# Optimization experiments

Hardware: AMD Instinct MI355X
Metric: run time of the kernel (lower is better)

The kernel has to match this reference:

```python
import jax, jax.numpy as jnp
import numpy as np

B = 128          # batch
H = 4            # input_size (number of local blocks / heads)
SEQ = 256        # seq_length
E = 64           # embedding_size
D = 64           # qkv_size
LH = SEQ // H    # seq_length_head = 64
NEG = -1e20

def setup_inputs() -> dict:
    key = jax.random.key(0)
    ks = jax.random.split(key, 7)
    scale = 0.02
    sequence = jax.random.normal(ks[0], (B, SEQ, E), dtype=jnp.float32)
    WQ = jax.random.normal(ks[1], (H, LH * D, LH * E), dtype=jnp.float32) * scale
    WK = jax.random.normal(ks[2], (H, LH * D, LH * E), dtype=jnp.float32) * scale
    WV = jax.random.normal(ks[3], (H, LH * D, LH * E), dtype=jnp.float32) * scale
    bQ = jax.random.normal(ks[4], (H, LH * D), dtype=jnp.float32) * scale
    bK = jax.random.normal(ks[5], (H, LH * D), dtype=jnp.float32) * scale
    bV = jax.random.normal(ks[6], (H, LH * D), dtype=jnp.float32) * scale
    return {"sequence": sequence, "WQ": WQ, "bQ": bQ, "WK": WK, "bK": bK, "WV": WV, "bV": bV}

def reference(sequence, WQ, bQ, WK, bK, WV, bV):
    b = sequence.shape[0]
    # split sequence into H independent local blocks, flatten each block
    x = sequence.reshape(b, H, LH * E)  # [B, H, Lh*E]
    # per-block dense projections (flattened linears, as in the original)
    Q = (jnp.einsum('bhi,hoi->bho', x, WQ) + bQ).reshape(b, H, LH, D)
    K = (jnp.einsum('bhi,hoi->bho', x, WK) + bK).reshape(b, H, LH, D)
    V = (jnp.einsum('bhi,hoi->bho', x, WV) + bV).reshape(b, H, LH, D)
    scores = jnp.einsum('bhqd,bhkd->bhqk', Q, K)  # [B, H, Lh, Lh]
    # masked=True: add -1e20 above the diagonal (as in torch.triu(..., diagonal=1))
    mask = jnp.triu(jnp.full((LH, LH), NEG, dtype=scores.dtype), k=1)
    scores = scores + mask
    # FAITHFUL to original: nn.Softmax(dim=1) on [B, Lh, Lh] -> softmax over QUERY axis
    attn = jax.nn.softmax(scores, axis=2)
    Z = jnp.einsum('bhqk,bhkd->bhqd', attn, V) * (1.0 / jnp.sqrt(jnp.float32(D)))
    return Z.reshape(b, SEQ, D)
```

## Files before the change

kernel.cpp:

```cpp
#include <hip/hip_runtime.h>

typedef _Float16 half8 __attribute__((ext_vector_type(8)));
typedef float floatx16 __attribute__((ext_vector_type(16)));

#define B_   128
#define H_   4
#define SEQ_ 256
#define E_   64
#define D_   64
#define LH_  64
#define IN_  (LH_*E_)
#define OUT_ (LH_*D_)
#define QKV_MAT_ELEMS (B_*H_*OUT_)

__global__ __launch_bounds__(256, 3) void qkv_gemm(
    const float* __restrict__ seq,
    const float* __restrict__ WQ, const float* __restrict__ bQ,
    const float* __restrict__ WK, const float* __restrict__ bK,
    const float* __restrict__ WV, const float* __restrict__ bV,
    _Float16* __restrict__ qkv)
{
    const int o0  = blockIdx.x * 64;
    const int h   = blockIdx.y;
    const int mat = blockIdx.z;
    const float* __restrict__ W    = (mat == 0) ? WQ : (mat == 1) ? WK : WV;
    const float* __restrict__ bias = (mat == 0) ? bQ : (mat == 1) ? bK : bV;

    __shared__ half8 Xs[128 * 8];
    __shared__ half8 Wt[64 * 8];

    const int t    = threadIdx.x;
    const int wave = t >> 6;
    const int lane = t & 63;
    const int lrow = lane & 31;
    const int kg   = lane >> 5;

    floatx16 acc0, acc1;
    #pragma unroll
    for (int i = 0; i < 16; ++i) { acc0[i] = 0.f; acc1[i] = 0.f; }

    const size_t wbase = (size_t)h * IN_ * OUT_;

    for (int kt = 0; kt < 64; ++kt) {
        const int k0 = kt * 64;
        #pragma unroll
        for (int i = 0; i < 4; ++i) {
            int lin = t + 256 * i;
            int r = lin >> 3, k8 = lin & 7;
            const float* src = seq + (size_t)r * (SEQ_*E_) + (size_t)h * IN_ + k0 + k8 * 8;
            float4 f0 = ((const float4*)src)[0];
            float4 f1 = ((const float4*)src)[1];
            half8 v;
            v[0] = (_Float16)f0.x; v[1] = (_Float16)f0.y;
            v[2] = (_Float16)f0.z; v[3] = (_Float16)f0.w;
            v[4] = (_Float16)f1.x; v[5] = (_Float16)f1.y;
            v[6] = (_Float16)f1.z; v[7] = (_Float16)f1.w;
            Xs[r * 8 + (k8 ^ (r & 7))] = v;
        }
        #pragma unroll
        for (int i = 0; i < 2; ++i) {
            int lin = t + 256 * i;
            int r = lin >> 3, k8 = lin & 7;
            const float* src = W + wbase + (size_t)(o0 + r) * IN_ + k0 + k8 * 8;
            float4 f0 = ((const float4*)src)[0];
            float4 f1 = ((const float4*)src)[1];
            half8 v;
            v[0] = (_Float16)f0.x; v[1] = (_Float16)f0.y;
            v[2] = (_Float16)f0.z; v[3] = (_Float16)f0.w;
            v[4] = (_Float16)f1.x; v[5] = (_Float16)f1.y;
            v[6] = (_Float16)f1.z; v[7] = (_Float16)f1.w;
            Wt[r * 8 + (k8 ^ (r & 7))] = v;
        }
        __syncthreads();

        const int arow = wave * 32 + lrow;
        #pragma unroll
        for (int s = 0; s < 4; ++s) {
            int k8i = s * 2 + kg;
            half8 a  = Xs[arow * 8 + (k8i ^ (arow & 7))];
            half8 b0 = Wt[lrow * 8 + (k8i ^ (lrow & 7))];
            half8 b1 = Wt[(lrow + 32) * 8 + (k8i ^ (lrow & 7))];
            acc0 = __builtin_amdgcn_mfma_f32_32x32x16_f16(a, b0, acc0, 0, 0, 0);
            acc1 = __builtin_amdgcn_mfma_f32_32x32x16_f16(a, b1, acc1, 0, 0, 0);
        }
        __syncthreads();
    }

    const float bv0 = bias[(size_t)h * OUT_ + o0 + lrow];
    const float bv1 = bias[(size_t)h * OUT_ + o0 + 32 + lrow];
    _Float16* dst = qkv + (size_t)mat * QKV_MAT_ELEMS;
    #pragma unroll
    for (int r = 0; r < 16; ++r) {
        int row = (r & 3) + 8 * (r >> 2) + 4 * kg;
        int b   = wave * 32 + row;
        size_t idx = ((size_t)(b * H_ + h)) * OUT_ + o0;
        dst[idx + lrow]      = (_Float16)(acc0[r] + bv0);
        dst[idx + 32 + lrow] = (_Float16)(acc1[r] + bv1);
    }
}

__global__ __launch_bounds__(256, 2) void local_attn(
    const _Float16* __restrict__ qkv, float* __restrict__ out)
{
    __shared__ float Qs[64 * 65];
    __shared__ float Ks[64 * 65];
    __shared__ float Vs[64 * 65];
    __shared__ float Ss[64 * 65];

    const int t = threadIdx.x;
    const int h = blockIdx.x;
    const int b = blockIdx.y;
    const size_t base = ((size_t)(b * H_ + h)) * OUT_;

    #pragma unroll
    for (int i = 0; i < 2; ++i) {
        int unit = t + 256 * i;
        int q = unit >> 3, d8 = unit & 7;
        half8 vq = *(const half8*)(qkv + base + q * 64 + d8 * 8);
        half8 vk = *(const half8*)(qkv + (size_t)QKV_MAT_ELEMS + base + q * 64 + d8 * 8);
        half8 vv = *(const half8*)(qkv + (size_t)2 * QKV_MAT_ELEMS + base + q * 64 + d8 * 8);
        #pragma unroll
        for (int j = 0; j < 8; ++j) {
            Qs[q * 65 + d8 * 8 + j] = (float)vq[j];
            Ks[q * 65 + d8 * 8 + j] = (float)vk[j];
            Vs[q * 65 + d8 * 8 + j] = (float)vv[j];
        }
    }
    __syncthreads();

    const int w = t >> 6, lane = t & 63;

    {
        float kr[64];
        #pragma unroll
        for (int d = 0; d < 64; ++d) kr[d] = Ks[lane * 65 + d];
        #pragma unroll 2
        for (int qi = 0; qi < 16; ++qi) {
            int q = w * 16 + qi;
            float s = 0.f;
            #pragma unroll
            for (int d = 0; d < 64; ++d) s += Qs[q * 65 + d] * kr[d];
            if (lane > q) s = -1e20f;
            Ss[q * 65 + lane] = s;
        }
    }
    __syncthreads();

    if (t < 64) {
        const int k = t;
        float m = -3.4e38f;
        for (int q = 0; q < 64; ++q) m = fmaxf(m, Ss[q * 65 + k]);
        float sum = 0.f;
        for (int q = 0; q < 64; ++q) {
            float e = __expf(Ss[q * 65 + k] - m);
            Ss[q * 65 + k] = e;
            sum += e;
        }
        float inv = 1.f / sum;
        for (int q = 0; q < 64; ++q) Ss[q * 65 + k] *= inv;
    }
    __syncthreads();

    {
        float vr[64];
        #pragma unroll
        for (int k = 0; k < 64; ++k) vr[k] = Vs[k * 65 + lane];
        #pragma unroll 2
        for (int qi = 0; qi < 16; ++qi) {
            int q = w * 16 + qi;
            float z = 0.f;
            #pragma unroll
            for (int k = 0; k < 64; ++k) z += Ss[q * 65 + k] * vr[k];
            out[((size_t)b * SEQ_ + h * LH_ + q) * D_ + lane] = z * 0.125f;
        }
    }
}

extern "C" void kernel_launch(void* const* d_in, const int* in_sizes, int n_in,
                              void* d_out, int out_size, void* d_ws, size_t ws_size,
                              hipStream_t stream)
{
    const float* seq = (const float*)d_in[0];
    const float* WQ  = (const float*)d_in[1];
    const float* bQ  = (const float*)d_in[2];
    const float* WK  = (const float*)d_in[3];
    const float* bK  = (const float*)d_in[4];
    const float* WV  = (const float*)d_in[5];
    const float* bV  = (const float*)d_in[6];
    _Float16* qkv = (_Float16*)d_ws;
    float* out = (float*)d_out;

    dim3 g1(64, H_, 3);
    qkv_gemm<<<g1, 256, 0, stream>>>(seq, WQ, bQ, WK, bK, WV, bV, qkv);
    dim3 g2(H_, B_);
    local_attn<<<g2, 256, 0, stream>>>(qkv, out);
}
```

Measured before the change: 805.9 us.

## Load GEMM operands directly to registers and use MFMA in local attention

New measurement: 956.1 us. 18.6% more time.

```diff
diff --git a/kernel.cpp b/kernel.cpp
--- a/kernel.cpp
+++ b/kernel.cpp
@@ -13,77 +13,68 @@
 #define OUT_ (LH_*D_)
 #define QKV_MAT_ELEMS (B_*H_*OUT_)
 
-__global__ __launch_bounds__(256, 3) void qkv_gemm(
+__device__ __forceinline__ half8 cvt8(float4 lo, float4 hi) {
+    half8 v;
+    v[0] = (_Float16)lo.x; v[1] = (_Float16)lo.y;
+    v[2] = (_Float16)lo.z; v[3] = (_Float16)lo.w;
+    v[4] = (_Float16)hi.x; v[5] = (_Float16)hi.y;
+    v[6] = (_Float16)hi.z; v[7] = (_Float16)hi.w;
+    return v;
+}
+
+__global__ __launch_bounds__(128) void qkv_gemm(
     const float* __restrict__ seq,
     const float* __restrict__ WQ, const float* __restrict__ bQ,
     const float* __restrict__ WK, const float* __restrict__ bK,
     const float* __restrict__ WV, const float* __restrict__ bV,
     _Float16* __restrict__ qkv)
 {
-    const int o0  = blockIdx.x * 64;
-    const int h   = blockIdx.y;
-    const int mat = blockIdx.z;
+    const int i   = blockIdx.x;
+    const int h   = (i >> 1) & 3;
+    const int sub = (i & 1) + ((i >> 3) << 1);
+    const int mat = sub >> 6;
+    const int nt  = sub & 63;
+    const int o0  = nt * 64;
+
     const float* __restrict__ W    = (mat == 0) ? WQ : (mat == 1) ? WK : WV;
     const float* __restrict__ bias = (mat == 0) ? bQ : (mat == 1) ? bK : bV;
 
-    __shared__ half8 Xs[128 * 8];
-    __shared__ half8 Wt[64 * 8];
-
-    const int t    = threadIdx.x;
-    const int wave = t >> 6;
-    const int lane = t & 63;
+    const int wave = threadIdx.x >> 6;
+    const int lane = threadIdx.x & 63;
     const int lrow = lane & 31;
     const int kg   = lane >> 5;
-
-    floatx16 acc0, acc1;
-    #pragma unroll
-    for (int i = 0; i < 16; ++i) { acc0[i] = 0.f; acc1[i] = 0.f; }
-
-    const size_t wbase = (size_t)h * IN_ * OUT_;
+    const int m0   = wave * 64;
+
+    const float* xr0 = seq + (size_t)(m0 + lrow) * (SEQ_*E_) + (size_t)h * IN_ + kg * 8;
+    const float* xr1 = xr0 + (size_t)32 * (SEQ_*E_);
+    const float* wr0 = W + (size_t)h * IN_ * OUT_ + (size_t)(o0 + lrow) * IN_ + kg * 8;
+    const float* wr1 = wr0 + (size_t)32 * IN_;
+
+    floatx16 acc00, acc01, acc10, acc11;
+    #pragma unroll
+    for (int r = 0; r < 16; ++r) { acc00[r]=0.f; acc01[r]=0.f; acc10[r]=0.f; acc11[r]=0.f; }
 
     for (int kt = 0; kt < 64; ++kt) {
-        const int k0 = kt * 64;
-        #pragma unroll
-        for (int i = 0; i < 4; ++i) {
-            int lin = t + 256 * i;
-            int r = lin >> 3, k8 = lin & 7;
-            const float* src = seq + (size_t)r * (SEQ_*E_) + (size_t)h * IN_ + k0 + k8 * 8;
-            float4 f0 = ((const float4*)src)[0];
-            float4 f1 = ((const float4*)src)[1];
-            half8 v;
-            v[0] = (_Float16)f0.x; v[1] = (_Float16)f0.y;
-            v[2] = (_Float16)f0.z; v[3] = (_Float16)f0.w;
-            v[4] = (_Float16)f1.x; v[5] = (_Float16)f1.y;
-            v[6] = (_Float16)f1.z; v[7] = (_Float16)f1.w;
-            Xs[r * 8 + (k8 ^ (r & 7))] = v;
-        }
-        #pragma unroll
-        for (int i = 0; i < 2; ++i) {
-            int lin = t + 256 * i;
-            int r = lin >> 3, k8 = lin & 7;
-            const float* src = W + wbase + (size_t)(o0 + r) * IN_ + k0 + k8 * 8;
-            float4 f0 = ((const float4*)src)[0];
-            float4 f1 = ((const float4*)src)[1];
-            half8 v;
-            v[0] = (_Float16)f0.x; v[1] = (_Float16)f0.y;
-            v[2] = (_Float16)f0.z; v[3] = (_Float16)f0.w;
-            v[4] = (_Float16)f1.x; v[5] = (_Float16)f1.y;
-            v[6] = (_Float16)f1.z; v[7] = (_Float16)f1.w;
-            Wt[r * 8 + (k8 ^ (r & 7))] = v;
-        }
-        __syncthreads();
-
-        const int arow = wave * 32 + lrow;
         #pragma unroll
         for (int s = 0; s < 4; ++s) {
-            int k8i = s * 2 + kg;
-            half8 a  = Xs[arow * 8 + (k8i ^ (arow & 7))];
-            half8 b0 = Wt[lrow * 8 + (k8i ^ (lrow & 7))];
-            half8 b1 = Wt[(lrow + 32) * 8 + (k8i ^ (lrow & 7))];
-            acc0 = __builtin_amdgcn_mfma_f32_32x32x16_f16(a, b0, acc0, 0, 0, 0);
-            acc1 = __builtin_amdgcn_mfma_f32_32x32x16_f16(a, b1, acc1, 0, 0, 0);
-        }
-        __syncthreads();
+            const int k = kt * 64 + s * 16;
+            float4 a0l = *(const float4*)(xr0 + k);
+            float4 a0h = *(const float4*)(xr0 + k + 4);
+            float4 a1l = *(const float4*)(xr1 + k);
+            float4 a1h = *(const float4*)(xr1 + k + 4);
+            float4 b0l = *(const float4*)(wr0 + k);
+            float4 b0h = *(const float4*)(wr0 + k + 4);
+            float4 b1l = *(const float4*)(wr1 + k);
+            float4 b1h = *(const float4*)(wr1 + k + 4);
+            half8 a0 = cvt8(a0l, a0h);
+            half8 a1 = cvt8(a1l, a1h);
+            half8 b0 = cvt8(b0l, b0h);
+            half8 b1 = cvt8(b1l, b1h);
+            acc00 = __builtin_amdgcn_mfma_f32_32x32x16_f16(a0, b0, acc00, 0, 0, 0);
+            acc01 = __builtin_amdgcn_mfma_f32_32x32x16_f16(a0, b1, acc01, 0, 0, 0);
+            acc10 = __builtin_amdgcn_mfma_f32_32x32x16_f16(a1, b0, acc10, 0, 0, 0);
+            acc11 = __builtin_amdgcn_mfma_f32_32x32x16_f16(a1, b1, acc11, 0, 0, 0);
+        }
     }
 
     const float bv0 = bias[(size_t)h * OUT_ + o0 + lrow];
@@ -91,88 +82,127 @@
     _Float16* dst = qkv + (size_t)mat * QKV_MAT_ELEMS;
     #pragma unroll
     for (int r = 0; r < 16; ++r) {
-        int row = (r & 3) + 8 * (r >> 2) + 4 * kg;
-        int b   = wave * 32 + row;
-        size_t idx = ((size_t)(b * H_ + h)) * OUT_ + o0;
-        dst[idx + lrow]      = (_Float16)(acc0[r] + bv0);
-        dst[idx + 32 + lrow] = (_Float16)(acc1[r] + bv1);
-    }
-}
-
-__global__ __launch_bounds__(256, 2) void local_attn(
+        const int row = (r & 3) + 8 * (r >> 2) + 4 * kg;
+        const int b0r = m0 + row;
+        const int b1r = m0 + 32 + row;
+        size_t i0 = ((size_t)(b0r * H_ + h)) * OUT_ + o0;
+        size_t i1 = ((size_t)(b1r * H_ + h)) * OUT_ + o0;
+        dst[i0 + lrow]      = (_Float16)(acc00[r] + bv0);
+        dst[i0 + 32 + lrow] = (_Float16)(acc01[r] + bv1);
+        dst[i1 + lrow]      = (_Float16)(acc10[r] + bv0);
+        dst[i1 + 32 + lrow] = (_Float16)(acc11[r] + bv1);
+    }
+}
+
+__global__ __launch_bounds__(256) void local_attn(
     const _Float16* __restrict__ qkv, float* __restrict__ out)
 {
-    __shared__ float Qs[64 * 65];
-    __shared__ float Ks[64 * 65];
-    __shared__ float Vs[64 * 65];
-    __shared__ float Ss[64 * 65];
+    __shared__ half8 Pf[64 * 8];
+    __shared__ half8 Vt[64 * 8];
+    __shared__ float redM[2][64];
+    __shared__ float redS[2][64];
+    __shared__ float invL[64];
 
     const int t = threadIdx.x;
     const int h = blockIdx.x;
     const int b = blockIdx.y;
     const size_t base = ((size_t)(b * H_ + h)) * OUT_;
 
-    #pragma unroll
-    for (int i = 0; i < 2; ++i) {
-        int unit = t + 256 * i;
-        int q = unit >> 3, d8 = unit & 7;
-        half8 vq = *(const half8*)(qkv + base + q * 64 + d8 * 8);
-        half8 vk = *(const half8*)(qkv + (size_t)QKV_MAT_ELEMS + base + q * 64 + d8 * 8);
-        half8 vv = *(const half8*)(qkv + (size_t)2 * QKV_MAT_ELEMS + base + q * 64 + d8 * 8);
+    const _Float16* Q = qkv + base;
+    const _Float16* K = qkv + (size_t)QKV_MAT_ELEMS + base;
+    const _Float16* V = qkv + (size_t)2 * QKV_MAT_ELEMS + base;
+
+    half8 v0 = *(const half8*)(V + (size_t)t * 8);
+    half8 v1 = *(const half8*)(V + (size_t)(t + 256) * 8);
+
+    const int wave = t >> 6, lane = t & 63;
+    const int lrow = lane & 31, kg = lane >> 5;
+    const int qt = wave >> 1, kt = wave & 1;
+
+    floatx16 s;
+    #pragma unroll
+    for (int r = 0; r < 16; ++r) s[r] = 0.f;
+    #pragma unroll
+    for (int st = 0; st < 4; ++st) {
+        half8 a  = *(const half8*)(Q + (qt * 32 + lrow) * 64 + st * 16 + kg * 8);
+        half8 bb = *(const half8*)(K + (kt * 32 + lrow) * 64 + st * 16 + kg * 8);
+        s = __builtin_amdgcn_mfma_f32_32x32x16_f16(a, bb, s, 0, 0, 0);
+    }
+
+    const int col = kt * 32 + lrow;
+    float m = -3.4e38f;
+    #pragma unroll
+    for (int r = 0; r < 16; ++r) {
+        const int q = qt * 32 + (r & 3) + 8 * (r >> 2) + 4 * kg;
+        if (col > q) s[r] = -1e20f;
+        m = fmaxf(m, s[r]);
+    }
+    m = fmaxf(m, __shfl_xor(m, 32));
+    redM[qt][col] = m;
+    __syncthreads();
+    m = fmaxf(redM[0][col], redM[1][col]);
+
+    float sum = 0.f;
+    #pragma unroll
+    for (int r = 0; r < 16; ++r) {
+        float e = __expf(s[r] - m);
+        s[r] = e;
+        sum += e;
+    }
+    sum += __shfl_xor(sum, 32);
+    redS[qt][col] = sum;
+    __syncthreads();
+    const float inv = 1.f / (redS[0][col] + redS[1][col]);
+    if (qt == 0 && kg == 0) invL[col] = inv * 0.125f;
+
+    {
+        _Float16* p = (_Float16*)Pf;
+        const int k8 = col >> 3;
+        #pragma unroll
+        for (int r = 0; r < 16; ++r) {
+            const int q = qt * 32 + (r & 3) + 8 * (r >> 2) + 4 * kg;
+            p[(q * 8 + (k8 ^ (q & 7))) * 8 + (col & 7)] = (_Float16)s[r];
+        }
+    }
+    __syncthreads();
+
+    {
+        _Float16* vt = (_Float16*)Vt;
+        const int k0 = t >> 3, d80 = t & 7;
+        const float iv0 = invL[k0];
         #pragma unroll
         for (int j = 0; j < 8; ++j) {
-            Qs[q * 65 + d8 * 8 + j] = (float)vq[j];
-            Ks[q * 65 + d8 * 8 + j] = (float)vk[j];
-            Vs[q * 65 + d8 * 8 + j] = (float)vv[j];
-        }
-    }
-    __syncthreads();
-
-    const int w = t >> 6, lane = t & 63;
-
-    {
-        float kr[64];
-        #pragma unroll
-        for (int d = 0; d < 64; ++d) kr[d] = Ks[lane * 65 + d];
-        #pragma unroll 2
-        for (int qi = 0; qi < 16; ++qi) {
-            int q = w * 16 + qi;
-            float s = 0.f;
-            #pragma unroll
-            for (int d = 0; d < 64; ++d) s += Qs[q * 65 + d] * kr[d];
-            if (lane > q) s = -1e20f;
-            Ss[q * 65 + lane] = s;
-        }
-    }
-    __syncthreads();
-
-    if (t < 64) {
-        const int k = t;
-        float m = -3.4e38f;
-        for (int q = 0; q < 64; ++q) m = fmaxf(m, Ss[q * 65 + k]);
-        float sum = 0.f;
-        for (int q = 0; q < 64; ++q) {
-            float e = __expf(Ss[q * 65 + k] - m);
-            Ss[q * 65 + k] = e;
-            sum += e;
-        }
-        float inv = 1.f / sum;
-        for (int q = 0; q < 64; ++q) Ss[q * 65 + k] *= inv;
-    }
-    __syncthreads();
-
-    {
-        float vr[64];
-        #pragma unroll
-        for (int k = 0; k < 64; ++k) vr[k] = Vs[k * 65 + lane];
-        #pragma unroll 2
-        for (int qi = 0; qi < 16; ++qi) {
-            int q = w * 16 + qi;
-            float z = 0.f;
-            #pragma unroll
-            for (int k = 0; k < 64; ++k) z += Ss[q * 65 + k] * vr[k];
-            out[((size_t)b * SEQ_ + h * LH_ + q) * D_ + lane] = z * 0.125f;
-        }
+            const int d = d80 * 8 + j;
+            vt[(d * 8 + ((k0 >> 3) ^ (d & 7))) * 8 + (k0 & 7)] = (_Float16)((float)v0[j] * iv0);
+        }
+        const int k1 = (t + 256) >> 3;
+        const float iv1 = invL[k1];
+        #pragma unroll
+        for (int j = 0; j < 8; ++j) {
+            const int d = d80 * 8 + j;
+            vt[(d * 8 + ((k1 >> 3) ^ (d & 7))) * 8 + (k1 & 7)] = (_Float16)((float)v1[j] * iv1);
+        }
+    }
+    __syncthreads();
+
+    const int dt = kt;
+    floatx16 z;
+    #pragma unroll
+    for (int r = 0; r < 16; ++r) z[r] = 0.f;
+    #pragma unroll
+    for (int st = 0; st < 4; ++st) {
+        const int k8 = st * 2 + kg;
+        const int q  = qt * 32 + lrow;
+        const int d  = dt * 32 + lrow;
+        half8 a  = Pf[q * 8 + (k8 ^ (q & 7))];
+        half8 bb = Vt[d * 8 + (k8 ^ (d & 7))];
+        z = __builtin_amdgcn_mfma_f32_32x32x16_f16(a, bb, z, 0, 0, 0);
+    }
+    #pragma unroll
+    for (int r = 0; r < 16; ++r) {
+        const int q = qt * 32 + (r & 3) + 8 * (r >> 2) + 4 * kg;
+        const int d = dt * 32 + lrow;
+        out[((size_t)b * SEQ_ + h * LH_ + q) * D_ + d] = z[r];
     }
 }
 
@@ -190,8 +220,7 @@
     _Float16* qkv = (_Float16*)d_ws;
     float* out = (float*)d_out;
 
-    dim3 g1(64, H_, 3);
-    qkv_gemm<<<g1, 256, 0, stream>>>(seq, WQ, bQ, WK, bK, WV, bV, qkv);
+    qkv_gemm<<<768, 128, 0, stream>>>(seq, WQ, bQ, WK, bK, WV, bV, qkv);
     dim3 g2(H_, B_);
     local_attn<<<g2, 256, 0, stream>>>(qkv, out);
 }
```
